# Kernel tuning notes

Measured on AMD Instinct MI355X. Metric: run time of the kernel, lower is better.

## Reference

```python
import jax, jax.numpy as jnp
import numpy as np

EMBED = 2048
HEADS = 16
HEAD_DIM = EMBED // HEADS


def setup_inputs() -> dict:
    key = jax.random.key(0)
    k1, k2 = jax.random.split(key)
    X = jax.random.normal(k1, (2, 2048, EMBED), dtype=jnp.float32)
    W_qkv = jax.random.normal(k2, (EMBED, 3 * EMBED), dtype=jnp.float32) * (1.0 / np.sqrt(EMBED))
    b_qkv = jnp.zeros((3 * EMBED,), dtype=jnp.float32)
    return {"X": X, "W_qkv": W_qkv, "b_qkv": b_qkv}


def reference(X, W_qkv, b_qkv):
    B, S, D = X.shape
    qkv = jnp.einsum('bsd,de->bse', X, W_qkv) + b_qkv  # [B,S,3D]
    q, k, v = jnp.split(qkv, 3, axis=-1)
    # [B,S,D] -> [B,H,S,hd]
    def heads(t):
        return t.reshape(B, S, HEADS, HEAD_DIM).transpose(0, 2, 1, 3)
    q, k, v = heads(q), heads(k), heads(v)
    scale = 1.0 / np.sqrt(HEAD_DIM).astype(np.float32)
    attention_score = jnp.einsum('bhqd,bhkd->bhqk', q, k) * scale
    scores = jax.nn.softmax(attention_score, axis=-1)  # [B,H,S,S]
    attention = jnp.einsum('bhqk,bhkd->bhqd', scores, v)
    attention = attention.transpose(0, 2, 1, 3).reshape(B, S, D)
    return (attention, scores)
```

## Files before the change

kernel.cpp:

```cpp
#include <hip/hip_runtime.h>
#include <hip/hip_bf16.h>

typedef __attribute__((ext_vector_type(8))) short short8;
typedef __attribute__((ext_vector_type(4))) float floatx4;

#define SEQ 2048
#define EMB 2048
#define NH 16
#define HD 128
#define E3 6144
#define SC2 0.12751224765383853f

static __device__ __forceinline__ unsigned short f2bf(float f) {
  unsigned u = __builtin_bit_cast(unsigned, f);
  u += 0x7fffu + ((u >> 16) & 1u);
  return (unsigned short)(u >> 16);
}

static __device__ __forceinline__ void gld_lds16(const unsigned short* g, unsigned short* l) {
  __builtin_amdgcn_global_load_lds(
      (const __attribute__((address_space(1))) void*)g,
      (__attribute__((address_space(3))) void*)l, 16, 0, 0);
}

__global__ void k_tx(const float* __restrict__ X, unsigned short* __restrict__ Xb) {
  long i = ((long)blockIdx.x * 256 + threadIdx.x) * 8;
  float4 f0 = *(const float4*)(X + i);
  float4 f1 = *(const float4*)(X + i + 4);
  uint4 u;
  u.x = (unsigned)f2bf(f0.x) | ((unsigned)f2bf(f0.y) << 16);
  u.y = (unsigned)f2bf(f0.z) | ((unsigned)f2bf(f0.w) << 16);
  u.z = (unsigned)f2bf(f1.x) | ((unsigned)f2bf(f1.y) << 16);
  u.w = (unsigned)f2bf(f1.z) | ((unsigned)f2bf(f1.w) << 16);
  *(uint4*)(Xb + i) = u;
}

__global__ void k_tw(const float* __restrict__ W, unsigned short* __restrict__ Wt) {
  __shared__ unsigned short t[32][33];
  int tx = threadIdx.x, ty = threadIdx.y;
  int e0 = blockIdx.x * 32, d0 = blockIdx.y * 32;
#pragma unroll
  for (int k = 0; k < 4; k++)
    t[ty + k * 8][tx] = f2bf(W[(long)(d0 + ty + k * 8) * E3 + e0 + tx]);
  __syncthreads();
#pragma unroll
  for (int k = 0; k < 4; k++)
    Wt[(long)(e0 + ty + k * 8) * EMB + d0 + tx] = t[tx][ty + k * 8];
}

__global__ void k_tv(const unsigned short* __restrict__ qkv, unsigned short* __restrict__ Vt) {
  __shared__ unsigned short t[32][33];
  int tx = threadIdx.x, ty = threadIdx.y;
  int z = blockIdx.z;
  int b = z >> 4, h = z & 15;
  int s0 = blockIdx.x * 32, d0 = blockIdx.y * 32;
#pragma unroll
  for (int k = 0; k < 4; k++) {
    int s = s0 + ty + k * 8;
    t[ty + k * 8][tx] = qkv[(long)(b * SEQ + s) * E3 + 2 * EMB + h * HD + d0 + tx];
  }
  __syncthreads();
#pragma unroll
  for (int k = 0; k < 4; k++) {
    int d = d0 + ty + k * 8;
    Vt[((long)z * HD + d) * SEQ + s0 + tx] = t[tx][ty + k * 8];
  }
}

__global__ __launch_bounds__(256) void k_proj(const unsigned short* __restrict__ Xb,
                                              const unsigned short* __restrict__ Wt,
                                              unsigned short* __restrict__ qkv,
                                              const float* __restrict__ bias) {
  __shared__ unsigned short As[128][64];
  __shared__ unsigned short Bs[128][64];

  int bid = blockIdx.x;
  int swz = (bid & 7) * 192 + (bid >> 3);
  int bx = swz % 48, by = swz / 48;
  long tM = (long)by * 128, tN = (long)bx * 128;

  int tid = threadIdx.x, lane = tid & 63, wave = tid >> 6;
  int wm = wave >> 1, wn = wave & 1, quad = lane >> 4, l16 = lane & 15;
  int lr = lane >> 3, lc = (lane & 7) * 8;

  const unsigned short* Ag = Xb + (tM + wave * 32 + lr) * EMB + lc;
  const unsigned short* Bg = Wt + (tN + wave * 32 + lr) * EMB + lc;

  floatx4 acc[4][4] = {};

  for (int k0 = 0; k0 < 2048; k0 += 64) {
#pragma unroll
    for (int c = 0; c < 4; c++) {
      gld_lds16(Ag + (long)(c * 8) * EMB + k0, &As[wave * 32 + c * 8][0]);
      gld_lds16(Bg + (long)(c * 8) * EMB + k0, &Bs[wave * 32 + c * 8][0]);
    }
    __syncthreads();
#pragma unroll
    for (int ks = 0; ks < 2; ks++) {
      short8 af[4], bfr[4];
#pragma unroll
      for (int i = 0; i < 4; i++)
        af[i] = *(const short8*)&As[wm * 64 + i * 16 + l16][ks * 32 + quad * 8];
#pragma unroll
      for (int j = 0; j < 4; j++)
        bfr[j] = *(const short8*)&Bs[wn * 64 + j * 16 + l16][ks * 32 + quad * 8];
#pragma unroll
      for (int i = 0; i < 4; i++)
#pragma unroll
        for (int j = 0; j < 4; j++)
          acc[i][j] = __builtin_amdgcn_mfma_f32_16x16x32_bf16(af[i], bfr[j], acc[i][j], 0, 0, 0);
    }
    __syncthreads();
  }

  float b4[4];
#pragma unroll
  for (int j = 0; j < 4; j++) b4[j] = bias[tN + wn * 64 + j * 16 + l16];

#pragma unroll
  for (int i = 0; i < 4; i++)
#pragma unroll
    for (int j = 0; j < 4; j++)
#pragma unroll
      for (int r = 0; r < 4; r++) {
        long row = tM + wm * 64 + i * 16 + quad * 4 + r;
        long col = tN + wn * 64 + j * 16 + l16;
        qkv[row * E3 + col] = f2bf(acc[i][j][r] + b4[j]);
      }
}

__global__ __launch_bounds__(256, 2) void k_attn(const unsigned short* __restrict__ qkv,
                                                 const unsigned short* __restrict__ Vt,
                                                 float* __restrict__ scores,
                                                 float* __restrict__ attn) {
  int id = blockIdx.x;
  int z = (id & 7) * 4 + ((id >> 3) >> 4);
  int qt = (id >> 3) & 15;
  int b = z >> 4, h = z & 15;

  const unsigned short* Qg = qkv + (long)b * SEQ * E3 + h * HD;
  const unsigned short* Kg = Qg + EMB;
  const unsigned short* Vg = Vt + (long)z * HD * SEQ;
  float* Sg = scores + (long)z * SEQ * SEQ + (long)qt * 128 * SEQ;
  float* Og = attn + (long)b * SEQ * EMB + (long)qt * 128 * EMB + h * HD;

  __shared__ unsigned short Kt[64][136];
  __shared__ unsigned short Vs[128][72];
  __shared__ unsigned short Ps[128][72];

  int tid = threadIdx.x;
  int lane = tid & 63, wave = tid >> 6;
  int quad = lane >> 4, l16 = lane & 15;

  short8 qf[2][4];
#pragma unroll
  for (int i = 0; i < 2; i++)
#pragma unroll
    for (int ks = 0; ks < 4; ks++)
      qf[i][ks] = *(const short8*)(Qg + (long)(qt * 128 + wave * 32 + i * 16 + l16) * E3 +
                                   ks * 32 + quad * 8);

  floatx4 oacc[2][8] = {};
  float rs[2][4] = {};

  uint4 kreg[4], vreg[4];
  auto loadK = [&](int t) {
#pragma unroll
    for (int c = 0; c < 4; c++) {
      int i2 = tid + 256 * c;
      kreg[c] = *(const uint4*)(Kg + (long)(t * 64 + (i2 >> 4)) * E3 + (i2 & 15) * 8);
    }
  };
  auto loadV = [&](int t) {
#pragma unroll
    for (int c = 0; c < 4; c++) {
      int i2 = tid + 256 * c;
      vreg[c] = *(const uint4*)(Vg + (long)(i2 >> 3) * SEQ + t * 64 + (i2 & 7) * 8);
    }
  };

  loadK(0);
  loadV(0);

  for (int t = 0; t < 32; t++) {
#pragma unroll
    for (int c = 0; c < 4; c++) {
      int i2 = tid + 256 * c;
      *(uint4*)&Kt[i2 >> 4][(i2 & 15) * 8] = kreg[c];
      *(uint4*)&Vs[i2 >> 3][(i2 & 7) * 8] = vreg[c];
    }
    __syncthreads();
    if (t < 31) { loadK(t + 1); loadV(t + 1); }

    floatx4 sacc[2][4] = {};
#pragma unroll
    for (int ks = 0; ks < 4; ks++) {
      short8 kf[4];
#pragma unroll
      for (int j = 0; j < 4; j++)
        kf[j] = *(const short8*)&Kt[j * 16 + l16][ks * 32 + quad * 8];
#pragma unroll
      for (int i = 0; i < 2; i++)
#pragma unroll
        for (int j = 0; j < 4; j++)
          sacc[i][j] = __builtin_amdgcn_mfma_f32_16x16x32_bf16(qf[i][ks], kf[j], sacc[i][j], 0, 0, 0);
    }
#pragma unroll
    for (int i = 0; i < 2; i++)
#pragma unroll
      for (int j = 0; j < 4; j++)
#pragma unroll
        for (int r = 0; r < 4; r++) {
          float e = exp2f(sacc[i][j][r] * SC2);
          rs[i][r] += e;
          Ps[wave * 32 + i * 16 + quad * 4 + r][j * 16 + l16] = f2bf(e);
        }
    __syncthreads();
#pragma unroll
    for (int ks = 0; ks < 2; ks++) {
      short8 pf[2], vf[8];
#pragma unroll
      for (int i = 0; i < 2; i++)
        pf[i] = *(const short8*)&Ps[wave * 32 + i * 16 + l16][ks * 32 + quad * 8];
#pragma unroll
      for (int j = 0; j < 8; j++)
        vf[j] = *(const short8*)&Vs[j * 16 + l16][ks * 32 + quad * 8];
#pragma unroll
      for (int i = 0; i < 2; i++)
#pragma unroll
        for (int j = 0; j < 8; j++)
          oacc[i][j] = __builtin_amdgcn_mfma_f32_16x16x32_bf16(pf[i], vf[j], oacc[i][j], 0, 0, 0);
    }
    __syncthreads();
  }

  loadK(0);

  float irs[2][4];
#pragma unroll
  for (int i = 0; i < 2; i++)
#pragma unroll
    for (int r = 0; r < 4; r++) {
      float s = rs[i][r];
      s += __shfl_xor(s, 1, 64);
      s += __shfl_xor(s, 2, 64);
      s += __shfl_xor(s, 4, 64);
      s += __shfl_xor(s, 8, 64);
      irs[i][r] = 1.0f / s;
    }

#pragma unroll
  for (int i = 0; i < 2; i++)
#pragma unroll
    for (int j = 0; j < 8; j++)
#pragma unroll
      for (int r = 0; r < 4; r++)
        Og[(long)(wave * 32 + i * 16 + quad * 4 + r) * EMB + j * 16 + l16] =
            oacc[i][j][r] * irs[i][r];

  for (int t = 0; t < 32; t++) {
#pragma unroll
    for (int c = 0; c < 4; c++) {
      int i2 = tid + 256 * c;
      *(uint4*)&Kt[i2 >> 4][(i2 & 15) * 8] = kreg[c];
    }
    __syncthreads();
    if (t < 31) loadK(t + 1);

    floatx4 sacc[2][4] = {};
#pragma unroll
    for (int ks = 0; ks < 4; ks++) {
      short8 kf[4];
#pragma unroll
      for (int j = 0; j < 4; j++)
        kf[j] = *(const short8*)&Kt[j * 16 + l16][ks * 32 + quad * 8];
#pragma unroll
      for (int i = 0; i < 2; i++)
#pragma unroll
        for (int j = 0; j < 4; j++)
          sacc[i][j] = __builtin_amdgcn_mfma_f32_16x16x32_bf16(qf[i][ks], kf[j], sacc[i][j], 0, 0, 0);
    }
#pragma unroll
    for (int i = 0; i < 2; i++)
#pragma unroll
      for (int j = 0; j < 4; j++)
#pragma unroll
        for (int r = 0; r < 4; r++)
          Sg[(long)(wave * 32 + i * 16 + quad * 4 + r) * SEQ + t * 64 + j * 16 + l16] =
              exp2f(sacc[i][j][r] * SC2) * irs[i][r];
    __syncthreads();
  }
}

extern "C" void kernel_launch(void* const* d_in, const int* in_sizes, int n_in,
                              void* d_out, int out_size, void* d_ws, size_t ws_size,
                              hipStream_t stream) {
  const float* X = (const float*)d_in[0];
  const float* W = (const float*)d_in[1];
  const float* bias = (const float*)d_in[2];
  float* out = (float*)d_out;
  float* attn = out;
  float* scores = out + (long)2 * SEQ * EMB;

  unsigned short* Wt = (unsigned short*)d_ws;
  unsigned short* qkv = Wt + (long)E3 * EMB;
  unsigned short* Vt = qkv + (long)2 * SEQ * E3;
  unsigned short* Xb = Vt;

  k_tx<<<dim3(4096), dim3(256), 0, stream>>>(X, Xb);
  k_tw<<<dim3(E3 / 32, EMB / 32), dim3(32, 8), 0, stream>>>(W, Wt);
  k_proj<<<dim3(1536), dim3(256), 0, stream>>>(Xb, Wt, qkv, bias);
  k_tv<<<dim3(SEQ / 32, HD / 32, 2 * NH), dim3(32, 8), 0, stream>>>(qkv, Vt);
  k_attn<<<dim3(512), dim3(256), 0, stream>>>(qkv, Vt, scores, attn);
}
```

Before: 1.155 ms.

## Halve attention query tile to 64 rows, swizzle LDS, raise occupancy

The attention kernel now processes 64 query rows per block instead of 128, so each wave handles 16 rows, and the grid doubles to 1024 blocks. Padded LDS arrays are replaced with XOR-swizzled layouts, which shrinks shared memory and aims to avoid bank conflicts. Launch bounds are raised to 4 blocks per CU for more occupancy. The cost is that each K/V tile is loaded twice as often relative to the compute done on it, which increases global and LDS traffic.

```diff
diff --git a/kernel.cpp b/kernel.cpp
--- a/kernel.cpp
+++ b/kernel.cpp
@@ -129,39 +129,40 @@
       }
 }
 
-__global__ __launch_bounds__(256, 2) void k_attn(const unsigned short* __restrict__ qkv,
+#define SWZK(row, col) ((((row) * 128) + (col)) ^ (((row) & 7) << 3))
+#define SWZ64(row, col) ((((row) * 64) + (col)) ^ (((row) & 7) << 3))
+
+__global__ __launch_bounds__(256, 4) void k_attn(const unsigned short* __restrict__ qkv,
                                                  const unsigned short* __restrict__ Vt,
                                                  float* __restrict__ scores,
                                                  float* __restrict__ attn) {
   int id = blockIdx.x;
-  int z = (id & 7) * 4 + ((id >> 3) >> 4);
-  int qt = (id >> 3) & 15;
+  int inner = id >> 3;
+  int z = (id & 7) * 4 + (inner >> 5);
+  int qt = inner & 31;
   int b = z >> 4, h = z & 15;
 
   const unsigned short* Qg = qkv + (long)b * SEQ * E3 + h * HD;
   const unsigned short* Kg = Qg + EMB;
   const unsigned short* Vg = Vt + (long)z * HD * SEQ;
-  float* Sg = scores + (long)z * SEQ * SEQ + (long)qt * 128 * SEQ;
-  float* Og = attn + (long)b * SEQ * EMB + (long)qt * 128 * EMB + h * HD;
-
-  __shared__ unsigned short Kt[64][136];
-  __shared__ unsigned short Vs[128][72];
-  __shared__ unsigned short Ps[128][72];
+  float* Sg = scores + (long)z * SEQ * SEQ + (long)qt * 64 * SEQ;
+  float* Og = attn + (long)b * SEQ * EMB + (long)qt * 64 * EMB + h * HD;
+
+  __shared__ unsigned short Kt[64 * 128];
+  __shared__ unsigned short Vs[128 * 64];
+  __shared__ unsigned short Ps[64 * 64];
 
   int tid = threadIdx.x;
   int lane = tid & 63, wave = tid >> 6;
   int quad = lane >> 4, l16 = lane & 15;
 
-  short8 qf[2][4];
-#pragma unroll
-  for (int i = 0; i < 2; i++)
-#pragma unroll
-    for (int ks = 0; ks < 4; ks++)
-      qf[i][ks] = *(const short8*)(Qg + (long)(qt * 128 + wave * 32 + i * 16 + l16) * E3 +
-                                   ks * 32 + quad * 8);
-
-  floatx4 oacc[2][8] = {};
-  float rs[2][4] = {};
+  short8 qf[4];
+#pragma unroll
+  for (int ks = 0; ks < 4; ks++)
+    qf[ks] = *(const short8*)(Qg + (long)(qt * 64 + wave * 16 + l16) * E3 + ks * 32 + quad * 8);
+
+  floatx4 oacc[8] = {};
+  float rs[4] = {};
 
   uint4 kreg[4], vreg[4];
   auto loadK = [&](int t) {
@@ -186,108 +187,91 @@
 #pragma unroll
     for (int c = 0; c < 4; c++) {
       int i2 = tid + 256 * c;
-      *(uint4*)&Kt[i2 >> 4][(i2 & 15) * 8] = kreg[c];
-      *(uint4*)&Vs[i2 >> 3][(i2 & 7) * 8] = vreg[c];
+      *(uint4*)&Kt[SWZK(i2 >> 4, (i2 & 15) * 8)] = kreg[c];
+      *(uint4*)&Vs[SWZ64(i2 >> 3, (i2 & 7) * 8)] = vreg[c];
     }
     __syncthreads();
     if (t < 31) { loadK(t + 1); loadV(t + 1); }
 
-    floatx4 sacc[2][4] = {};
+    floatx4 sacc[4] = {};
 #pragma unroll
     for (int ks = 0; ks < 4; ks++) {
       short8 kf[4];
 #pragma unroll
       for (int j = 0; j < 4; j++)
-        kf[j] = *(const short8*)&Kt[j * 16 + l16][ks * 32 + quad * 8];
-#pragma unroll
-      for (int i = 0; i < 2; i++)
-#pragma unroll
-        for (int j = 0; j < 4; j++)
-          sacc[i][j] = __builtin_amdgcn_mfma_f32_16x16x32_bf16(qf[i][ks], kf[j], sacc[i][j], 0, 0, 0);
-    }
-#pragma unroll
-    for (int i = 0; i < 2; i++)
-#pragma unroll
-      for (int j = 0; j < 4; j++)
-#pragma unroll
-        for (int r = 0; r < 4; r++) {
-          float e = exp2f(sacc[i][j][r] * SC2);
-          rs[i][r] += e;
-          Ps[wave * 32 + i * 16 + quad * 4 + r][j * 16 + l16] = f2bf(e);
-        }
+        kf[j] = *(const short8*)&Kt[SWZK(j * 16 + l16, ks * 32 + quad * 8)];
+#pragma unroll
+      for (int j = 0; j < 4; j++)
+        sacc[j] = __builtin_amdgcn_mfma_f32_16x16x32_bf16(qf[ks], kf[j], sacc[j], 0, 0, 0);
+    }
+#pragma unroll
+    for (int j = 0; j < 4; j++)
+#pragma unroll
+      for (int r = 0; r < 4; r++) {
+        float e = exp2f(sacc[j][r] * SC2);
+        rs[r] += e;
+        Ps[SWZ64(wave * 16 + quad * 4 + r, j * 16 + l16)] = f2bf(e);
+      }
     __syncthreads();
 #pragma unroll
     for (int ks = 0; ks < 2; ks++) {
-      short8 pf[2], vf[8];
-#pragma unroll
-      for (int i = 0; i < 2; i++)
-        pf[i] = *(const short8*)&Ps[wave * 32 + i * 16 + l16][ks * 32 + quad * 8];
+      short8 pf, vf[8];
+      pf = *(const short8*)&Ps[SWZ64(wave * 16 + l16, ks * 32 + quad * 8)];
 #pragma unroll
       for (int j = 0; j < 8; j++)
-        vf[j] = *(const short8*)&Vs[j * 16 + l16][ks * 32 + quad * 8];
-#pragma unroll
-      for (int i = 0; i < 2; i++)
-#pragma unroll
-        for (int j = 0; j < 8; j++)
-          oacc[i][j] = __builtin_amdgcn_mfma_f32_16x16x32_bf16(pf[i], vf[j], oacc[i][j], 0, 0, 0);
+        vf[j] = *(const short8*)&Vs[SWZ64(j * 16 + l16, ks * 32 + quad * 8)];
+#pragma unroll
+      for (int j = 0; j < 8; j++)
+        oacc[j] = __builtin_amdgcn_mfma_f32_16x16x32_bf16(pf, vf[j], oacc[j], 0, 0, 0);
     }
     __syncthreads();
   }
 
   loadK(0);
 
-  float irs[2][4];
-#pragma unroll
-  for (int i = 0; i < 2; i++)
-#pragma unroll
-    for (int r = 0; r < 4; r++) {
-      float s = rs[i][r];
-      s += __shfl_xor(s, 1, 64);
-      s += __shfl_xor(s, 2, 64);
-      s += __shfl_xor(s, 4, 64);
-      s += __shfl_xor(s, 8, 64);
-      irs[i][r] = 1.0f / s;
-    }
-
-#pragma unroll
-  for (int i = 0; i < 2; i++)
+  float irs[4];
+#pragma unroll
+  for (int r = 0; r < 4; r++) {
+    float s = rs[r];
+    s += __shfl_xor(s, 1, 64);
+    s += __shfl_xor(s, 2, 64);
+    s += __shfl_xor(s, 4, 64);
+    s += __shfl_xor(s, 8, 64);
+    irs[r] = 1.0f / s;
+  }
+
+#pragma unroll
+  for (int r = 0; r < 4; r++)
 #pragma unroll
     for (int j = 0; j < 8; j++)
-#pragma unroll
-      for (int r = 0; r < 4; r++)
-        Og[(long)(wave * 32 + i * 16 + quad * 4 + r) * EMB + j * 16 + l16] =
-            oacc[i][j][r] * irs[i][r];
+      Og[(long)(wave * 16 + quad * 4 + r) * EMB + j * 16 + l16] = oacc[j][r] * irs[r];
 
   for (int t = 0; t < 32; t++) {
 #pragma unroll
     for (int c = 0; c < 4; c++) {
       int i2 = tid + 256 * c;
-      *(uint4*)&Kt[i2 >> 4][(i2 & 15) * 8] = kreg[c];
+      *(uint4*)&Kt[SWZK(i2 >> 4, (i2 & 15) * 8)] = kreg[c];
     }
     __syncthreads();
     if (t < 31) loadK(t + 1);
 
-    floatx4 sacc[2][4] = {};
+    floatx4 sacc[4] = {};
 #pragma unroll
     for (int ks = 0; ks < 4; ks++) {
       short8 kf[4];
 #pragma unroll
       for (int j = 0; j < 4; j++)
-        kf[j] = *(const short8*)&Kt[j * 16 + l16][ks * 32 + quad * 8];
-#pragma unroll
-      for (int i = 0; i < 2; i++)
-#pragma unroll
-        for (int j = 0; j < 4; j++)
-          sacc[i][j] = __builtin_amdgcn_mfma_f32_16x16x32_bf16(qf[i][ks], kf[j], sacc[i][j], 0, 0, 0);
-    }
-#pragma unroll
-    for (int i = 0; i < 2; i++)
-#pragma unroll
-      for (int j = 0; j < 4; j++)
-#pragma unroll
-        for (int r = 0; r < 4; r++)
-          Sg[(long)(wave * 32 + i * 16 + quad * 4 + r) * SEQ + t * 64 + j * 16 + l16] =
-              exp2f(sacc[i][j][r] * SC2) * irs[i][r];
+        kf[j] = *(const short8*)&Kt[SWZK(j * 16 + l16, ks * 32 + quad * 8)];
+#pragma unroll
+      for (int j = 0; j < 4; j++)
+        sacc[j] = __builtin_amdgcn_mfma_f32_16x16x32_bf16(qf[ks], kf[j], sacc[j], 0, 0, 0);
+    }
+#pragma unroll
+    for (int r = 0; r < 4; r++)
+#pragma unroll
+      for (int j = 0; j < 4; j++)
+        Sg[(long)(wave * 16 + quad * 4 + r) * SEQ + t * 64 + j * 16 + l16] =
+            exp2f(sacc[j][r] * SC2) * irs[r];
     __syncthreads();
   }
 }
@@ -311,5 +295,5 @@
   k_tw<<<dim3(E3 / 32, EMB / 32), dim3(32, 8), 0, stream>>>(W, Wt);
   k_proj<<<dim3(1536), dim3(256), 0, stream>>>(Xb, Wt, qkv, bias);
   k_tv<<<dim3(SEQ / 32, HD / 32, 2 * NH), dim3(32, 8), 0, stream>>>(qkv, Vt);
-  k_attn<<<dim3(512), dim3(256), 0, stream>>>(qkv, Vt, scores, attn);
-}
+  k_attn<<<dim3(1024), dim3(256), 0, stream>>>(qkv, Vt, scores, attn);
+}
```

New measurement: 1.512 ms. 1.31x slower.
